# Performance work log

Measured on AMD Instinct MI355X. Metric: run time of the kernel, lower is better.

## Reference

```python
import jax, jax.numpy as jnp
import numpy as np


def setup_inputs() -> dict:
    key = jax.random.key(0)
    ks = jax.random.split(key, 6)
    T, B, I, H = 256, 64, 1024, 1024
    x = jax.random.normal(ks[0], (T, B, I), dtype=jnp.float32)
    h0 = jax.random.normal(ks[1], (B, H), dtype=jnp.float32)
    c0 = jax.random.normal(ks[2], (B, H), dtype=jnp.float32)
    # LSTMCell params: _W [I+H, 4H] (xavier-like scale), _b zeros
    W = jax.random.normal(ks[3], (I + H, 4 * H), dtype=jnp.float32) * (2.0 / (I + H + 4 * H)) ** 0.5
    b = jnp.zeros((4 * H,), dtype=jnp.float32)
    L = jax.random.randint(ks[4], (B,), 0, T, dtype=jnp.int64 if jax.config.jax_enable_x64 else jnp.int32)
    return {"x": x, "h0": h0, "c0": c0, "W": W, "b": b, "L": L}


def reference(x, h0, c0, W, b, L):
    # RNN(cell_type='lstm', num_layers=1, batch_first=False) forward.
    # x: [T, B, I]; h0, c0: [B, H]; W: [I+H, 4H]; b: [4H]; L: [B] lengths.
    T = x.shape[0]
    H = h0.shape[-1]

    def step(carry, inp):
        h_, c_ = carry
        xt, t = inp  # xt: [B, I]
        cand = jnp.concatenate([xt, h_], axis=-1) @ W + b  # [B, 4H]
        i, f, o, g = jnp.split(cand, 4, axis=-1)
        c_new = jax.nn.sigmoid(i) * jnp.tanh(g) + jax.nn.sigmoid(f) * c_
        h_new = jax.nn.sigmoid(o) * jnp.tanh(c_new)
        mask = (t < L)[:, None]  # [B, 1]; freeze state past sequence end
        h = jnp.where(mask, h_new, h_)
        c = jnp.where(mask, c_new, c_)
        return (h, c), h

    (_, _), out = jax.lax.scan(step, (h0, c0), (x, jnp.arange(T)))
    return out  # [T, B, H]
```

## Files before the change

kernel.cpp:

```cpp
#include <hip/hip_runtime.h>
#include <stdint.h>

typedef unsigned short u16;
typedef unsigned int u32;
typedef unsigned long long u64;
typedef __attribute__((ext_vector_type(8))) short bf16x8;
typedef __attribute__((ext_vector_type(4))) float f32x4;
typedef __attribute__((ext_vector_type(4))) u16 u16x4;
typedef __attribute__((ext_vector_type(2))) u64 u64x2;

#define T_STEPS 256
#define BATCH 64
#define IDIM 1024
#define HDIM 1024
#define NBLK 256
#define NJ 4
#define KPAD 2056
#define THREADS 512
#define FLAG_LINE_U32 16
#define GO_U32 (NBLK * FLAG_LINE_U32)
#define X_OFF 262144
#define H_OFF (X_OFF + T_STEPS * BATCH * IDIM * 2)
#define LDS_BYTES 83712

static __device__ __forceinline__ u16 f2bf(float f) {
  u32 u = __builtin_bit_cast(u32, f);
  u += 0x7FFFu + ((u >> 16) & 1u);
  return (u16)(u >> 16);
}
static __device__ __forceinline__ float sigf(float x) {
  return __builtin_amdgcn_rcpf(1.f + __expf(-x));
}
static __device__ __forceinline__ float tanhf_(float x) {
  float ax = __builtin_fabsf(x);
  float e = __expf(-2.f * ax);
  float t = 1.f - 2.f * e * __builtin_amdgcn_rcpf(1.f + e);
  return __builtin_copysignf(t, x);
}

static __device__ __forceinline__ void gwait(u32* flags, u32* go, u32 e,
                                             int bid, int tid, int lane) {
  if (bid == 0) {
    if ((tid >> 6) == 7) {
      const u32* p0 = &flags[lane * FLAG_LINE_U32];
      const u32* p1 = &flags[(lane + 64) * FLAG_LINE_U32];
      const u32* p2 = &flags[(lane + 128) * FLAG_LINE_U32];
      const u32* p3 = &flags[(lane + 192) * FLAG_LINE_U32];
      while (true) {
        u32 a = __hip_atomic_load(p0, __ATOMIC_RELAXED, __HIP_MEMORY_SCOPE_AGENT);
        u32 b = __hip_atomic_load(p1, __ATOMIC_RELAXED, __HIP_MEMORY_SCOPE_AGENT);
        u32 c = __hip_atomic_load(p2, __ATOMIC_RELAXED, __HIP_MEMORY_SCOPE_AGENT);
        u32 d = __hip_atomic_load(p3, __ATOMIC_RELAXED, __HIP_MEMORY_SCOPE_AGENT);
        int mine = (a >= e) && (b >= e) && (c >= e) && (d >= e);
        if (__all(mine)) break;
        __builtin_amdgcn_s_sleep(1);
      }
      if (lane < 8)
        __hip_atomic_store(&go[lane * FLAG_LINE_U32], e, __ATOMIC_RELAXED,
                           __HIP_MEMORY_SCOPE_AGENT);
    }
  } else {
    if (tid == 448) {
      while (__hip_atomic_load(&go[(bid & 7) * FLAG_LINE_U32], __ATOMIC_RELAXED,
                               __HIP_MEMORY_SCOPE_AGENT) < e)
        __builtin_amdgcn_s_sleep(2);
    }
  }
  if (tid == 448)
    __builtin_amdgcn_fence(__ATOMIC_ACQUIRE, "agent");
  __syncthreads();
}

static __device__ __forceinline__ void gbar_heavy(u32* flags, u32* go, int bid,
                                                  int tid) {
  __syncthreads();
  if (tid == 0) {
    __threadfence();
    __hip_atomic_store(&flags[bid * FLAG_LINE_U32], 1u, __ATOMIC_RELAXED,
                       __HIP_MEMORY_SCOPE_AGENT);
  }
  if (bid == 0) {
    if (tid < NBLK) {
      while (__hip_atomic_load(&flags[tid * FLAG_LINE_U32], __ATOMIC_RELAXED,
                               __HIP_MEMORY_SCOPE_AGENT) < 1u)
        __builtin_amdgcn_s_sleep(1);
    }
    __syncthreads();
    if (tid < 8)
      __hip_atomic_store(&go[tid * FLAG_LINE_U32], 1u, __ATOMIC_RELAXED,
                         __HIP_MEMORY_SCOPE_AGENT);
  } else {
    if (tid == 0) {
      while (__hip_atomic_load(&go[(bid & 7) * FLAG_LINE_U32], __ATOMIC_RELAXED,
                               __HIP_MEMORY_SCOPE_AGENT) < 1u)
        __builtin_amdgcn_s_sleep(2);
    }
  }
  if (tid == 0) __threadfence();
  __syncthreads();
}

__global__ __launch_bounds__(THREADS, 2)
void lstm_persistent(const float* __restrict__ x, const float* __restrict__ h0,
                     const float* __restrict__ c0, const float* __restrict__ W,
                     const float* __restrict__ bias, const int* __restrict__ L,
                     float* __restrict__ out, u16* __restrict__ xbf,
                     u16* __restrict__ hbuf, u32* __restrict__ flags) {
  extern __shared__ char smem[];
  u16* Wlds = (u16*)smem;
  float* cand = (float*)(smem + 65792);
  u16* hstage = (u16*)(smem + 83200);

  u32* go = flags + GO_U32;

  const int bid = blockIdx.x;
  const int tid = threadIdx.x;
  const int wave = tid >> 6;
  const int lane = tid & 63;
  const int q = lane >> 4;
  const int ln = lane & 15;
  const int mh = wave & 1;
  const int kq = wave >> 1;
  const int arow = 32 * mh + ln;

  {
    const int gtid = bid * THREADS + tid;
    const f32x4* xv = (const f32x4*)x;
    u16x4* ov = (u16x4*)xbf;
#pragma unroll
    for (int it = 0; it < 32; ++it) {
      int i = gtid + it * (NBLK * THREADS);
      f32x4 v = xv[i];
      u16x4 o;
      o[0] = f2bf(v[0]); o[1] = f2bf(v[1]); o[2] = f2bf(v[2]); o[3] = f2bf(v[3]);
      ov[i] = o;
    }
    if (gtid < BATCH * HDIM) {
      int b = gtid >> 10, j = gtid & 1023;
      hbuf[BATCH * HDIM + (j >> 2) * 256 + b * 4 + (j & 3)] = f2bf(h0[gtid]);
    }
  }

  {
    const int g = tid & 3;
    const int kq2 = tid >> 2;
    const f32x4* Wv = (const f32x4*)W;
#pragma unroll 4
    for (int i = 0; i < 16; ++i) {
      int k = kq2 + 128 * i;
      f32x4 w4 = Wv[(size_t)k * 1024 + g * 256 + bid];
#pragma unroll
      for (int jj = 0; jj < 4; ++jj)
        Wlds[(g * 4 + jj) * KPAD + k] = f2bf(w4[jj]);
    }
  }

  float c_reg = 0.f, h_reg = 0.f, b_i = 0.f, b_f = 0.f, b_o = 0.f, b_g = 0.f;
  int Lb = 0, pb = 0, pj = 0;
  if (tid < 256) {
    pb = tid >> 2;
    pj = tid & 3;
    int gj = bid * NJ + pj;
    Lb = L[pb];
    c_reg = c0[pb * HDIM + gj];
    h_reg = h0[pb * HDIM + gj];
    b_i = bias[0 * HDIM + gj];
    b_f = bias[1 * HDIM + gj];
    b_o = bias[2 * HDIM + gj];
    b_g = bias[3 * HDIM + gj];
  }

  gbar_heavy(flags, go, bid, tid);

  const u16* wpx = &Wlds[ln * KPAD + kq * 256 + q * 8];
  const u16* wph = &Wlds[ln * KPAD + 1024 + kq * 256 + q * 8];

  for (int t = 0; t < T_STEPS; ++t) {
    f32x4 acc0 = {0.f, 0.f, 0.f, 0.f};
    f32x4 acc1 = {0.f, 0.f, 0.f, 0.f};
    {
      const u16* pa0 =
          xbf + (size_t)t * (BATCH * IDIM) + arow * 1024 + kq * 256 + q * 8;
      const u16* pa1 = pa0 + 16 * 1024;
#pragma unroll
      for (int ks = 0; ks < 8; ++ks) {
        bf16x8 a0 = *(const bf16x8*)(pa0 + ks * 32);
        bf16x8 a1 = *(const bf16x8*)(pa1 + ks * 32);
        bf16x8 bw = *(const bf16x8*)(wpx + ks * 32);
        acc0 = __builtin_amdgcn_mfma_f32_16x16x32_bf16(a0, bw, acc0, 0, 0, 0);
        acc1 = __builtin_amdgcn_mfma_f32_16x16x32_bf16(a1, bw, acc1, 0, 0, 0);
      }
    }
    asm volatile("" ::"v"(acc0), "v"(acc1));
    __builtin_amdgcn_sched_barrier(0);

    if (t > 0) gwait(flags, go, (u32)(t + 1), bid, tid, lane);

    {
      const u16* hb = hbuf + ((t + 1) & 1) * (BATCH * HDIM) + kq * (256 * 64) +
                      q * (2 * 256);
#pragma unroll
      for (int ks = 0; ks < 8; ++ks) {
        const u16* c0p_ = hb + ks * (8 * 256);
        u64x2 r0, r1;
        r0[0] = *(const u64*)(c0p_ + arow * 4);
        r0[1] = *(const u64*)(c0p_ + 256 + arow * 4);
        r1[0] = *(const u64*)(c0p_ + (arow + 16) * 4);
        r1[1] = *(const u64*)(c0p_ + 256 + (arow + 16) * 4);
        bf16x8 a0 = __builtin_bit_cast(bf16x8, r0);
        bf16x8 a1 = __builtin_bit_cast(bf16x8, r1);
        bf16x8 bw = *(const bf16x8*)(wph + ks * 32);
        acc0 = __builtin_amdgcn_mfma_f32_16x16x32_bf16(a0, bw, acc0, 0, 0, 0);
        acc1 = __builtin_amdgcn_mfma_f32_16x16x32_bf16(a1, bw, acc1, 0, 0, 0);
      }
    }
    {
      float* c0p = &cand[(wave * 32 + q * 4) * 17 + ln];
      float* c1p = c0p + 16 * 17;
#pragma unroll
      for (int r = 0; r < 4; ++r) {
        c0p[r * 17] = acc0[r];
        c1p[r * 17] = acc1[r];
      }
    }
    __syncthreads();
    if (tid < 256) {
      const int mhp = pb >> 5, lr = pb & 31;
      float vi = b_i, vf = b_f, vo = b_o, vg = b_g;
#pragma unroll
      for (int p = 0; p < 4; ++p) {
        const float* cp = &cand[((p * 2 + mhp) * 32 + lr) * 17];
        vi += cp[pj];
        vf += cp[4 + pj];
        vo += cp[8 + pj];
        vg += cp[12 + pj];
      }
      float ig = sigf(vi), fg = sigf(vf), og = sigf(vo), gg = tanhf_(vg);
      float cn = ig * gg + fg * c_reg;
      float hn = og * tanhf_(cn);
      if (t < Lb) { c_reg = cn; h_reg = hn; }
      hstage[tid] = f2bf(h_reg);
    }
    __syncthreads();
    if (t < T_STEPS - 1) {
      if (tid < 64) {
        u64 v = ((const u64*)hstage)[tid];
        u64* dst =
            (u64*)(hbuf + (t & 1) * (BATCH * HDIM) + bid * 256 + tid * 4);
        __hip_atomic_store(dst, v, __ATOMIC_RELAXED, __HIP_MEMORY_SCOPE_AGENT);
      }
      __syncthreads();
      if (tid == 0)
        __hip_atomic_store(&flags[bid * FLAG_LINE_U32], (u32)(t + 2),
                           __ATOMIC_RELAXED, __HIP_MEMORY_SCOPE_AGENT);
    }
    if (tid < 256)
      __hip_atomic_store(&out[((size_t)t * BATCH + pb) * HDIM + bid * NJ + pj],
                         h_reg, __ATOMIC_RELAXED, __HIP_MEMORY_SCOPE_AGENT);
  }
}

extern "C" void kernel_launch(void* const* d_in, const int* in_sizes, int n_in,
                              void* d_out, int out_size, void* d_ws, size_t ws_size,
                              hipStream_t stream) {
  (void)in_sizes; (void)n_in; (void)out_size; (void)ws_size;
  const float* x = (const float*)d_in[0];
  const float* h0 = (const float*)d_in[1];
  const float* c0 = (const float*)d_in[2];
  const float* W = (const float*)d_in[3];
  const float* bias = (const float*)d_in[4];
  const int* L = (const int*)d_in[5];
  float* out = (float*)d_out;

  char* ws = (char*)d_ws;
  u32* flags = (u32*)ws;
  u16* xbf = (u16*)(ws + X_OFF);
  u16* hbuf = (u16*)(ws + H_OFF);

  hipFuncSetAttribute(reinterpret_cast<const void*>(lstm_persistent),
                      hipFuncAttributeMaxDynamicSharedMemorySize, 160 * 1024);
  hipMemsetAsync(ws, 0, 32768, stream);
  hipLaunchKernelGGL(lstm_persistent, dim3(NBLK), dim3(THREADS), LDS_BYTES,
                     stream, x, h0, c0, W, bias, L, out, xbf, hbuf, flags);
}
```

Baseline: 2.478 ms.

## Pack h via shuffles, signal per-wave LDS counter, and re-layout W in LDS

```diff
diff --git a/kernel.cpp b/kernel.cpp
--- a/kernel.cpp
+++ b/kernel.cpp
@@ -15,13 +15,14 @@
 #define HDIM 1024
 #define NBLK 256
 #define NJ 4
-#define KPAD 2056
 #define THREADS 512
 #define FLAG_LINE_U32 16
 #define GO_U32 (NBLK * FLAG_LINE_U32)
 #define X_OFF 262144
 #define H_OFF (X_OFF + T_STEPS * BATCH * IDIM * 2)
-#define LDS_BYTES 83712
+#define CAND_OFF 65536
+#define CNT_OFF (CAND_OFF + 17408)
+#define LDS_BYTES (CNT_OFF + 64)
 
 static __device__ __forceinline__ u16 f2bf(float f) {
   u32 u = __builtin_bit_cast(u32, f);
@@ -108,8 +109,8 @@
                      u16* __restrict__ hbuf, u32* __restrict__ flags) {
   extern __shared__ char smem[];
   u16* Wlds = (u16*)smem;
-  float* cand = (float*)(smem + 65792);
-  u16* hstage = (u16*)(smem + 83200);
+  float* cand = (float*)(smem + CAND_OFF);
+  u32* cnt = (u32*)(smem + CNT_OFF);
 
   u32* go = flags + GO_U32;
 
@@ -123,6 +124,8 @@
   const int kq = wave >> 1;
   const int arow = 32 * mh + ln;
 
+  if (tid == 0) *cnt = 0;
+
   {
     const int gtid = bid * THREADS + tid;
     const f32x4* xv = (const f32x4*)x;
@@ -149,9 +152,11 @@
     for (int i = 0; i < 16; ++i) {
       int k = kq2 + 128 * i;
       f32x4 w4 = Wv[(size_t)k * 1024 + g * 256 + bid];
+      int kb = (k >> 5) * 64 + ((k >> 3) & 3) * 16;
+      int ko = k & 7;
 #pragma unroll
       for (int jj = 0; jj < 4; ++jj)
-        Wlds[(g * 4 + jj) * KPAD + k] = f2bf(w4[jj]);
+        Wlds[(kb + g * 4 + jj) * 8 + ko] = f2bf(w4[jj]);
     }
   }
 
@@ -172,8 +177,8 @@
 
   gbar_heavy(flags, go, bid, tid);
 
-  const u16* wpx = &Wlds[ln * KPAD + kq * 256 + q * 8];
-  const u16* wph = &Wlds[ln * KPAD + 1024 + kq * 256 + q * 8];
+  const u16* wpx = Wlds + ((size_t)(kq * 8) * 64 + lane) * 8;
+  const u16* wph = Wlds + ((size_t)(32 + kq * 8) * 64 + lane) * 8;
 
   for (int t = 0; t < T_STEPS; ++t) {
     f32x4 acc0 = {0.f, 0.f, 0.f, 0.f};
@@ -186,7 +191,7 @@
       for (int ks = 0; ks < 8; ++ks) {
         bf16x8 a0 = *(const bf16x8*)(pa0 + ks * 32);
         bf16x8 a1 = *(const bf16x8*)(pa1 + ks * 32);
-        bf16x8 bw = *(const bf16x8*)(wpx + ks * 32);
+        bf16x8 bw = *(const bf16x8*)(wpx + ks * 512);
         acc0 = __builtin_amdgcn_mfma_f32_16x16x32_bf16(a0, bw, acc0, 0, 0, 0);
         acc1 = __builtin_amdgcn_mfma_f32_16x16x32_bf16(a1, bw, acc1, 0, 0, 0);
       }
@@ -209,7 +214,7 @@
         r1[1] = *(const u64*)(c0p_ + 256 + (arow + 16) * 4);
         bf16x8 a0 = __builtin_bit_cast(bf16x8, r0);
         bf16x8 a1 = __builtin_bit_cast(bf16x8, r1);
-        bf16x8 bw = *(const bf16x8*)(wph + ks * 32);
+        bf16x8 bw = *(const bf16x8*)(wph + ks * 512);
         acc0 = __builtin_amdgcn_mfma_f32_16x16x32_bf16(a0, bw, acc0, 0, 0, 0);
         acc1 = __builtin_amdgcn_mfma_f32_16x16x32_bf16(a1, bw, acc1, 0, 0, 0);
       }
@@ -239,24 +244,28 @@
       float cn = ig * gg + fg * c_reg;
       float hn = og * tanhf_(cn);
       if (t < Lb) { c_reg = cn; h_reg = hn; }
-      hstage[tid] = f2bf(h_reg);
-    }
-    __syncthreads();
-    if (t < T_STEPS - 1) {
-      if (tid < 64) {
-        u64 v = ((const u64*)hstage)[tid];
-        u64* dst =
-            (u64*)(hbuf + (t & 1) * (BATCH * HDIM) + bid * 256 + tid * 4);
-        __hip_atomic_store(dst, v, __ATOMIC_RELAXED, __HIP_MEMORY_SCOPE_AGENT);
-      }
-      __syncthreads();
-      if (tid == 0)
-        __hip_atomic_store(&flags[bid * FLAG_LINE_U32], (u32)(t + 2),
-                           __ATOMIC_RELAXED, __HIP_MEMORY_SCOPE_AGENT);
-    }
-    if (tid < 256)
+      if (t < T_STEPS - 1) {
+        u32 v32 = (u32)f2bf(h_reg);
+        u32 a32 = v32 | (((u32)__shfl_xor((int)v32, 1)) << 16);
+        u32 b32 = (u32)__shfl_xor((int)a32, 2);
+        if ((tid & 3) == 0) {
+          u64 hw = (u64)a32 | ((u64)b32 << 32);
+          u64* hdst =
+              (u64*)(hbuf + (t & 1) * (BATCH * HDIM) + bid * 256) + pb;
+          __hip_atomic_store(hdst, hw, __ATOMIC_RELAXED,
+                             __HIP_MEMORY_SCOPE_AGENT);
+        }
+        asm volatile("s_waitcnt vmcnt(0)" ::: "memory");
+        if (lane == 0) {
+          u32 old = atomicAdd(cnt, 1u);
+          if ((old & 3) == 3)
+            __hip_atomic_store(&flags[bid * FLAG_LINE_U32], (u32)(t + 2),
+                               __ATOMIC_RELAXED, __HIP_MEMORY_SCOPE_AGENT);
+        }
+      }
       __hip_atomic_store(&out[((size_t)t * BATCH + pb) * HDIM + bid * NJ + pj],
                          h_reg, __ATOMIC_RELAXED, __HIP_MEMORY_SCOPE_AGENT);
+    }
   }
 }
 
```

Measured after the change: 2.224 ms. 10.2% less time.
